# Kernel tuning notes

Measured on AMD Instinct MI355X. Metric: run time of the kernel, lower is better.

The kernel has to match this reference:

```python
import jax, jax.numpy as jnp
import numpy as np

EMBED_DIM = 1024
NUM_HEADS = 16
N_POS = 2048
BATCH = 4


def setup_inputs() -> dict:
    key = jax.random.key(0)
    k_x, k_w1, k_b1, k_wo, k_bo = jax.random.split(key, 5)
    s1 = 1.0 / np.sqrt(EMBED_DIM)
    x = jax.random.normal(k_x, (BATCH, N_POS, EMBED_DIM), dtype=jnp.float32)
    # torch Linear weights stored as [in, out] for x @ W + b
    W_qkv = jax.random.uniform(k_w1, (EMBED_DIM, 3 * EMBED_DIM), dtype=jnp.float32, minval=-s1, maxval=s1)
    b_qkv = jax.random.uniform(k_b1, (3 * EMBED_DIM,), dtype=jnp.float32, minval=-s1, maxval=s1)
    W_o = jax.random.uniform(k_wo, (EMBED_DIM, EMBED_DIM), dtype=jnp.float32, minval=-s1, maxval=s1)
    b_o = jax.random.uniform(k_bo, (EMBED_DIM,), dtype=jnp.float32, minval=-s1, maxval=s1)
    return {"x": x, "W_qkv": W_qkv, "b_qkv": b_qkv, "W_o": W_o, "b_o": b_o}


def reference(x, W_qkv, b_qkv, W_o, b_o):
    B, N, C = x.shape
    H = NUM_HEADS
    d_k = C // H
    qkv = x @ W_qkv + b_qkv                       # [B, N, 3C]
    q, k, v = jnp.split(qkv, 3, axis=-1)
    q = q.reshape(B, N, H, d_k).transpose(0, 2, 1, 3)  # [B, H, N, d_k]
    k = k.reshape(B, N, H, d_k).transpose(0, 2, 1, 3)
    v = v.reshape(B, N, H, d_k).transpose(0, 2, 1, 3)
    scores = jnp.einsum('bhqd,bhkd->bhqk', q, k) * (1.0 / np.sqrt(d_k))
    causal = jnp.tril(jnp.ones((N, N), dtype=bool))
    scores = jnp.where(causal, scores, -jnp.inf)
    attn = jax.nn.softmax(scores, axis=-1)
    out = jnp.einsum('bhqk,bhkd->bhqd', attn, v)  # [B, H, N, d_k]
    out = out.transpose(0, 2, 1, 3).reshape(B, N, C)
    return out @ W_o + b_o
```

## Files before the change

### kernel.cpp

```cpp
#include <hip/hip_runtime.h>
#include <hip/hip_bf16.h>

typedef __attribute__((ext_vector_type(8))) __bf16 bf16x8;
typedef __attribute__((ext_vector_type(4))) float f32x4;
typedef __attribute__((ext_vector_type(16))) float f32x16;
typedef __attribute__((ext_vector_type(4))) unsigned short u16x4;
typedef __attribute__((ext_vector_type(8))) unsigned short u16x8;
typedef __attribute__((ext_vector_type(4))) unsigned int u32x4;
typedef unsigned short u16;

#define MFMA16 __builtin_amdgcn_mfma_f32_16x16x32_bf16
#define MFMA32 __builtin_amdgcn_mfma_f32_32x32x16_bf16

#if __has_builtin(__builtin_amdgcn_exp2f)
#define EXP2F __builtin_amdgcn_exp2f
#else
#define EXP2F(x) __expf((x) * 0.69314718056f)
#endif

__device__ inline u16 f32_to_bf16_bits(float f) {
    unsigned u = __builtin_bit_cast(unsigned, f);
    unsigned r = u + 0x7FFFu + ((u >> 16) & 1u);
    return (u16)(r >> 16);
}

__device__ inline void g2l16(const void* g, void* l) {
    __builtin_amdgcn_global_load_lds(
        (const __attribute__((address_space(1))) unsigned int*)g,
        (__attribute__((address_space(3))) unsigned int*)l,
        16, 0, 0);
}

__device__ inline float red32_max(float x) { return fmaxf(x, __shfl_xor(x, 32)); }
__device__ inline float red32_sum(float x) { return x + __shfl_xor(x, 32); }

__global__ void cvt_bf16_kernel(const float* __restrict__ in, u16* __restrict__ out, int n) {
    int i = (blockIdx.x * 256 + threadIdx.x) * 8;
    if (i >= n) return;
    f32x4 v0 = *(const f32x4*)&in[i];
    f32x4 v1 = *(const f32x4*)&in[i + 4];
    u16x8 r;
#pragma unroll
    for (int j = 0; j < 4; ++j) {
        r[j] = f32_to_bf16_bits(v0[j]);
        r[j + 4] = f32_to_bf16_bits(v1[j]);
    }
    *(u16x8*)&out[i] = r;
}

__global__ __launch_bounds__(256) void cvt_t2_kernel(
    const float* __restrict__ W1, u16* __restrict__ WT1, int N1,
    const float* __restrict__ W2, u16* __restrict__ WT2, int N2, int K)
{
    int bx = blockIdx.x;
    const float* W; u16* WT; int N;
    const int nb1 = N1 >> 6;
    if (bx < nb1) { W = W1; WT = WT1; N = N1; }
    else          { W = W2; WT = WT2; N = N2; bx -= nb1; }
    const int w = threadIdx.x >> 6, l = threadIdx.x & 63;
    const int n = bx * 64 + l;
    const int k0 = blockIdx.y * 32 + w * 8;
    u16x8 r;
#pragma unroll
    for (int i = 0; i < 8; ++i)
        r[i] = f32_to_bf16_bits(W[(size_t)(k0 + i) * N + n]);
    *(u16x8*)&WT[(size_t)n * K + k0] = r;
}

template <int STORE_BF16>
__global__ __launch_bounds__(256) void gemm_nt(
    const u16* __restrict__ A, const u16* __restrict__ BT,
    const float* __restrict__ bias, void* __restrict__ Cv,
    int M, int N, int K, int qcols, float qscale, int nbx)
{
    __shared__ __align__(16) u16 SM[24576];
    const int tid = threadIdx.x;
    const int w = tid >> 6, l = tid & 63;
    const int lr = l & 15, lh = l >> 4;
    const int wr = (w >> 1) * 64, wc = (w & 1) * 64;

    const int xcd = blockIdx.x & 7;
    const int j = blockIdx.x >> 3;
    const int g = j >> 5;
    const int r = j & 31;
    const int m0 = (xcd * 8 + (r >> 2)) * 128;
    const int n0 = (g * 4 + (r & 3)) * 128;
    (void)nbx;

    const int NT = K >> 5;

    const int f0 = tid, f1 = 256 + tid;
    const int r0 = f0 >> 2, r1 = f1 >> 2;
    const int cs0 = ((f0 & 3) ^ ((r0 >> 1) & 3)) * 8;
    const int cs1 = ((f1 & 3) ^ ((r1 >> 1) & 3)) * 8;
    const size_t arow0 = (size_t)(m0 + r0) * K, arow1 = (size_t)(m0 + r1) * K;
    const size_t brow0 = (size_t)(n0 + r0) * K, brow1 = (size_t)(n0 + r1) * K;

#define STAGE_TILE(t, set)                                                     \
    do {                                                                       \
        const int kk_ = (t) * 32;                                              \
        u16* dst_ = SM + (set) * 8192 + w * 512;                               \
        g2l16(A + arow0 + kk_ + cs0, dst_);                                    \
        g2l16(BT + brow0 + kk_ + cs0, dst_ + 4096);                            \
        g2l16(A + arow1 + kk_ + cs1, dst_ + 2048);                             \
        g2l16(BT + brow1 + kk_ + cs1, dst_ + 4096 + 2048);                     \
    } while (0)

    f32x4 acc[4][4];
#pragma unroll
    for (int m = 0; m < 4; ++m)
#pragma unroll
        for (int n = 0; n < 4; ++n) acc[m][n] = (f32x4)(0.0f);

    STAGE_TILE(0, 0);
    STAGE_TILE(1, 1);
    asm volatile("s_waitcnt vmcnt(4) lgkmcnt(0)\n\ts_barrier" ::: "memory");

    const int csw = (lr >> 1) & 3;
    int s0 = 0, s2 = 2;
    for (int t = 0; t < NT; ++t) {
        if (t + 2 < NT) STAGE_TILE(t + 2, s2);

        const u16* As = SM + s0 * 8192;
        const u16* Bs = As + 4096;
        bf16x8 af[4], bfr[4];
#pragma unroll
        for (int m = 0; m < 4; ++m)
            af[m] = *(const bf16x8*)&As[(wr + m * 16 + lr) * 32 + ((lh ^ csw) << 3)];
#pragma unroll
        for (int n = 0; n < 4; ++n)
            bfr[n] = *(const bf16x8*)&Bs[(wc + n * 16 + lr) * 32 + ((lh ^ csw) << 3)];
        __builtin_amdgcn_s_setprio(1);
#pragma unroll
        for (int m = 0; m < 4; ++m)
#pragma unroll
            for (int n = 0; n < 4; ++n)
                acc[m][n] = MFMA16(af[m], bfr[n], acc[m][n], 0, 0, 0);
        __builtin_amdgcn_s_setprio(0);

        if (t + 2 < NT)
            asm volatile("s_waitcnt vmcnt(4) lgkmcnt(0)\n\ts_barrier" ::: "memory");
        else if (t + 1 < NT)
            asm volatile("s_waitcnt vmcnt(0) lgkmcnt(0)\n\ts_barrier" ::: "memory");

        s0 = (s0 == 2) ? 0 : s0 + 1;
        s2 = (s2 == 2) ? 0 : s2 + 1;
    }
#undef STAGE_TILE

#pragma unroll
    for (int m = 0; m < 4; ++m) {
        int row = m0 + wr + m * 16 + lh * 4;
#pragma unroll
        for (int n = 0; n < 4; ++n) {
            int col = n0 + wc + n * 16 + lr;
            float bs = bias[col];
            float sc = (col < qcols) ? qscale : 1.0f;
#pragma unroll
            for (int j2 = 0; j2 < 4; ++j2) {
                float v = (acc[m][n][j2] + bs) * sc;
                if (STORE_BF16)
                    ((u16*)Cv)[(size_t)(row + j2) * N + col] = f32_to_bf16_bits(v);
                else
                    ((float*)Cv)[(size_t)(row + j2) * N + col] = v;
            }
        }
    }
}

__global__ __launch_bounds__(512, 1) void attn_kernel(
    const u16* __restrict__ qkv, u16* __restrict__ ctx)
{
    __shared__ __align__(16) u16 SM[32768];

    const int bid = blockIdx.x;
    const int xcd = bid & 7, jj = bid >> 3;
    const int bh = xcd * 8 + (jj >> 2);
    const int pr = jj & 3;
    const int b = bh >> 4, h = bh & 15;
    const size_t rowbase = (size_t)b * 2048;
    const int tid = threadIdx.x, w = tid >> 6, l = tid & 63;
    const int lq = l & 31, lk = l >> 5;

    const int rsub = l >> 3;
    const int cstage = l & 7;
    const int kchunk = cstage ^ rsub;

    bf16x8 vreg[2];

#pragma unroll
    for (int pass = 0; pass < 2; ++pass) {
        const int qt = pass ? (7 - pr) : pr;
        const int q0 = qt * 256;
        const int nt = 2 * qt + 2;
        const int qbase = q0 + w * 32;

        const u16* qp = qkv + (rowbase + qbase + lq) * 3072 + h * 64 + lk * 8;
        bf16x8 qf[4];
#pragma unroll
        for (int j = 0; j < 4; ++j) qf[j] = *(const bf16x8*)(qp + j * 16);

        f32x16 ot[2];
#pragma unroll
        for (int dt = 0; dt < 2; ++dt) ot[dt] = (f32x16)(0.0f);
        float m_run = -3e38f, l_run = 0.0f;

        __syncthreads();
#pragma unroll
        for (int p = 0; p < 2; ++p) {
            const int r = w * 16 + p * 8 + rsub;
            g2l16(qkv + (rowbase + r) * 3072 + 1024 + h * 64 + kchunk * 8,
                  SM + w * 1024 + p * 512);
            vreg[p] = *(const bf16x8*)(qkv + (rowbase + r) * 3072 + 2048 + h * 64 + cstage * 8);
        }
        asm volatile("s_waitcnt vmcnt(0)" ::: "memory");
#pragma unroll
        for (int p = 0; p < 2; ++p) {
            const int r = w * 16 + p * 8 + rsub;
#pragma unroll
            for (int i = 0; i < 8; ++i) {
                const int d = cstage * 8 + i;
                SM[16384 + ((d * 128 + r) ^ (((i ^ cstage) & 7) << 3))] = ((const u16*)&vreg[p])[i];
            }
        }
        __syncthreads();

        for (int t = 0; t < nt; ++t) {
            const int c = t & 1;
            const int kb = t * 128;
            u16* const Kb = SM + (c ? 8192 : 0);
            u16* const Vb = SM + 16384 + (c ? 8192 : 0);

            if (t + 1 < nt) {
                const int kb2 = kb + 128;
#pragma unroll
                for (int p = 0; p < 2; ++p) {
                    const int r = w * 16 + p * 8 + rsub;
                    g2l16(qkv + (rowbase + kb2 + r) * 3072 + 1024 + h * 64 + kchunk * 8,
                          SM + (c ? 0 : 8192) + w * 1024 + p * 512);
                    vreg[p] = *(const bf16x8*)(qkv + (rowbase + kb2 + r) * 3072 + 2048 + h * 64 + cstage * 8);
                }
            }

            if (kb <= qbase + 31) {
                bf16x8 kf[4][4];
#pragma unroll
                for (int kt = 0; kt < 4; ++kt)
#pragma unroll
                    for (int j = 0; j < 4; ++j)
                        kf[kt][j] = *(const bf16x8*)&Kb[((kt * 32 + lq) * 64 + j * 16 + lk * 8) ^ ((lq & 7) << 3)];

                f32x16 sf[4];
                __builtin_amdgcn_s_setprio(1);
#pragma unroll
                for (int kt = 0; kt < 4; ++kt) {
                    f32x16 z = (f32x16)(0.0f);
#pragma unroll
                    for (int j = 0; j < 4; ++j) z = MFMA32(kf[kt][j], qf[j], z, 0, 0, 0);
                    sf[kt] = z;
                }
                __builtin_amdgcn_s_setprio(0);

                float mt = -3e38f;
                if (kb + 127 > qbase) {
                    const int qrow = qbase + lq;
#pragma unroll
                    for (int kt = 0; kt < 4; ++kt)
#pragma unroll
                        for (int r = 0; r < 16; ++r) {
                            const int key = kb + kt * 32 + (r & 3) + 8 * (r >> 2) + 4 * lk;
                            float v = sf[kt][r];
                            if (key > qrow) v = -3e38f;
                            sf[kt][r] = v;
                            mt = fmaxf(mt, v);
                        }
                } else {
#pragma unroll
                    for (int kt = 0; kt < 4; ++kt)
#pragma unroll
                        for (int r = 0; r < 16; ++r) mt = fmaxf(mt, sf[kt][r]);
                }
                mt = red32_max(mt);

                const bool defer = __all(mt <= m_run + 16.0f);
                float mn = m_run;
                if (!defer) {
                    mn = fmaxf(m_run, mt);
                    const float alpha = EXP2F(m_run - mn);
                    m_run = mn;
                    l_run *= alpha;
#pragma unroll
                    for (int dt = 0; dt < 2; ++dt)
#pragma unroll
                        for (int r = 0; r < 16; ++r) ot[dt][r] *= alpha;
                }
                float rs = 0.0f;
#pragma unroll
                for (int kt = 0; kt < 4; ++kt)
#pragma unroll
                    for (int r = 0; r < 16; ++r) {
                        const float pp = EXP2F(sf[kt][r] - mn);
                        sf[kt][r] = pp;
                        rs += pp;
                    }
                l_run += red32_sum(rs);

                unsigned pc[4][4][2];
#pragma unroll
                for (int kt = 0; kt < 4; ++kt)
#pragma unroll
                    for (int rg = 0; rg < 4; ++rg) {
                        unsigned d0, d1;
                        asm("v_cvt_pk_bf16_f32 %0, %1, %2"
                            : "=v"(d0) : "v"((float)sf[kt][rg * 4 + 0]), "v"((float)sf[kt][rg * 4 + 1]));
                        asm("v_cvt_pk_bf16_f32 %0, %1, %2"
                            : "=v"(d1) : "v"((float)sf[kt][rg * 4 + 2]), "v"((float)sf[kt][rg * 4 + 3]));
                        pc[kt][rg][0] = d0;
                        pc[kt][rg][1] = d1;
                    }

                __builtin_amdgcn_s_setprio(1);
#pragma unroll
                for (int kt = 0; kt < 4; ++kt)
#pragma unroll
                    for (int hh = 0; hh < 2; ++hh) {
                        unsigned a0 = pc[kt][2 * hh][0], a1 = pc[kt][2 * hh][1];
                        unsigned b0 = pc[kt][2 * hh + 1][0], b1 = pc[kt][2 * hh + 1][1];
                        asm("v_permlane32_swap_b32 %0, %1" : "+v"(a0), "+v"(b0));
                        asm("v_permlane32_swap_b32 %0, %1" : "+v"(a1), "+v"(b1));
                        u32x4 wv = {a0, a1, b0, b1};
                        const bf16x8 pb = __builtin_bit_cast(bf16x8, wv);
                        const int k0 = 2 * kt + hh;
#pragma unroll
                        for (int dt = 0; dt < 2; ++dt) {
                            const int d = dt * 32 + lq;
                            const int vswz = ((d & 7) ^ (d >> 3)) & 7;
                            const bf16x8 vf = *(const bf16x8*)&Vb[((d * 128) + (k0 * 16 + lk * 8)) ^ (vswz << 3)];
                            ot[dt] = MFMA32(vf, pb, ot[dt], 0, 0, 0);
                        }
                    }
                __builtin_amdgcn_s_setprio(0);
            }

            asm volatile("s_waitcnt vmcnt(0)" ::: "memory");
            if (t + 1 < nt) {
                u16* const Vn = SM + 16384 + (c ? 0 : 8192);
#pragma unroll
                for (int p = 0; p < 2; ++p) {
                    const int r = w * 16 + p * 8 + rsub;
#pragma unroll
                    for (int i = 0; i < 8; ++i) {
                        const int d = cstage * 8 + i;
                        Vn[((d * 128 + r) ^ (((i ^ cstage) & 7) << 3))] = ((const u16*)&vreg[p])[i];
                    }
                }
            }
            __syncthreads();
        }

        u16* const out_l = SM + w * 2176;
        const float inv = 1.0f / l_run;
#pragma unroll
        for (int dt = 0; dt < 2; ++dt)
#pragma unroll
            for (int r = 0; r < 16; ++r) {
                const int d = dt * 32 + (r & 3) + 8 * (r >> 2) + 4 * lk;
                out_l[lq * 68 + d] = f32_to_bf16_bits(ot[dt][r] * inv);
            }
#pragma unroll
        for (int rr = 0; rr < 4; ++rr) {
            const int row = rr * 8 + (l >> 3);
            const bf16x8 v = *(const bf16x8*)&out_l[row * 68 + (l & 7) * 8];
            *(bf16x8*)(ctx + (rowbase + qbase + row) * 1024 + h * 64 + (l & 7) * 8) = v;
        }
    }
}

extern "C" void kernel_launch(void* const* d_in, const int* in_sizes, int n_in,
                              void* d_out, int out_size, void* d_ws, size_t ws_size,
                              hipStream_t stream) {
    const float* x      = (const float*)d_in[0];
    const float* W_qkv  = (const float*)d_in[1];
    const float* b_qkv  = (const float*)d_in[2];
    const float* W_o    = (const float*)d_in[3];
    const float* b_o    = (const float*)d_in[4];
    float* out = (float*)d_out;

    const int M = 4 * 2048;
    const int C = 1024;
    u16* qkv   = (u16*)d_ws;
    u16* xb    = qkv   + (size_t)M * 3 * C;
    u16* wqkvt = xb    + (size_t)M * C;
    u16* ctx   = wqkvt + (size_t)3 * C * C;
    u16* wot   = ctx   + (size_t)M * C;

    const float SCQ = 0.125f * 1.44269504089f;

    cvt_bf16_kernel<<<(M * C) / (256 * 8), 256, 0, stream>>>(x, xb, M * C);
    cvt_t2_kernel<<<dim3(3 * C / 64 + C / 64, C / 32), 256, 0, stream>>>(
        W_qkv, wqkvt, 3 * C, W_o, wot, C, C);

    gemm_nt<1><<<(3 * C / 128) * (M / 128), 256, 0, stream>>>(xb, wqkvt, b_qkv, qkv,
                                                              M, 3 * C, C, C, SCQ, 3 * C / 128);

    attn_kernel<<<256, 512, 0, stream>>>(qkv, ctx);

    gemm_nt<0><<<(C / 128) * (M / 128), 256, 0, stream>>>(ctx, wot, b_o, out,
                                                          M, C, C, 0, 1.0f, C / 128);
}
```

Baseline: 161.9 us.

## Add 8-wave 128x256 tiled GEMM with chunked staging for QKV projection

Adds a new QKV projection GEMM that uses 512 threads (8 waves) and a 128x256 output tile, double-buffered in 96KB of LDS. Global-to-LDS copies are split into three chunks that are interleaved with two MFMA phases, with explicit barriers and wave priority bumps around the MFMA blocks. The wider N tile is meant to increase reuse of the A tile and reduce global traffic, while the pipelining hides load latency. The cost is more LDS per block and extra barriers, which may lower occupancy.

```diff
diff --git a/kernel.cpp b/kernel.cpp
--- a/kernel.cpp
+++ b/kernel.cpp
@@ -68,6 +68,134 @@
 }
 
 template <int STORE_BF16>
+__global__ __launch_bounds__(512) void gemm_8p2(
+    const u16* __restrict__ A, const u16* __restrict__ BT,
+    const float* __restrict__ bias, void* __restrict__ Cv,
+    int M, int N, int K, int qcols, float qscale)
+{
+    __shared__ __align__(16) u16 SM[49152];
+    const int tid = threadIdx.x;
+    const int w = tid >> 6, l = tid & 63;
+    const int lr = l & 15, lh = l >> 4;
+    const int wr = (w >> 2) * 64;
+    const int wc = (w & 3) * 64;
+
+    const int xcd = blockIdx.x & 7;
+    const int jb = blockIdx.x >> 3;
+    const int g = jb >> 4;
+    const int r = jb & 15;
+    const int m0 = (xcd * 8 + (r >> 1)) * 128;
+    const int n0 = (g * 2 + (r & 1)) * 256;
+
+    const int NT = K >> 6;
+
+    const int f0 = tid, f1 = 512 + tid;
+    const int r0 = f0 >> 3, r1 = f1 >> 3;
+    const int c0 = ((f0 & 7) ^ (r0 & 7)) * 8;
+
+#define STAGE_CHUNK(j, c)                                                       \
+    do {                                                                        \
+        const int kk_ = (j) * 64;                                               \
+        u16* db_ = SM + (((j) & 1) * 24576) + (c) * 8192;                       \
+        const u16* base_ = ((c) == 0) ? (A + (size_t)m0 * K)                    \
+                                      : (BT + (size_t)(n0 + ((c)-1) * 128) * K);\
+        g2l16(base_ + (size_t)r0 * K + kk_ + c0, db_ + f0 * 8);                 \
+        g2l16(base_ + (size_t)r1 * K + kk_ + c0, db_ + f1 * 8);                 \
+    } while (0)
+
+    f32x4 acc[4][4];
+#pragma unroll
+    for (int m = 0; m < 4; ++m)
+#pragma unroll
+        for (int n = 0; n < 4; ++n) acc[m][n] = (f32x4)(0.0f);
+
+    STAGE_CHUNK(0, 0); STAGE_CHUNK(0, 1); STAGE_CHUNK(0, 2);
+
+    const int swk = lr & 7;
+    for (int j = 0; j < NT; ++j) {
+        const u16* Ab = SM + (j & 1) * 24576;
+        const u16* Bb = Ab + 8192;
+
+        if (j + 1 < NT) {
+            STAGE_CHUNK(j + 1, 0);
+            asm volatile("s_waitcnt vmcnt(2)\n\ts_barrier" ::: "memory");
+        } else {
+            asm volatile("s_waitcnt vmcnt(0)\n\ts_barrier" ::: "memory");
+        }
+
+        bf16x8 af[4][2], bfr[2][2];
+#pragma unroll
+        for (int m = 0; m < 4; ++m) {
+            const int row = wr + m * 16 + lr;
+#pragma unroll
+            for (int ks = 0; ks < 2; ++ks)
+                af[m][ks] = *(const bf16x8*)&Ab[row * 64 + (((ks * 4 + lh) ^ swk) << 3)];
+        }
+#pragma unroll
+        for (int n = 0; n < 2; ++n) {
+            const int row = wc + n * 16 + lr;
+#pragma unroll
+            for (int ks = 0; ks < 2; ++ks)
+                bfr[n][ks] = *(const bf16x8*)&Bb[row * 64 + (((ks * 4 + lh) ^ swk) << 3)];
+        }
+        if (j + 1 < NT) STAGE_CHUNK(j + 1, 1);
+
+        asm volatile("s_barrier\n\ts_waitcnt lgkmcnt(0)" ::: "memory");
+        __builtin_amdgcn_s_setprio(1);
+#pragma unroll
+        for (int m = 0; m < 4; ++m)
+#pragma unroll
+            for (int n = 0; n < 2; ++n)
+#pragma unroll
+                for (int ks = 0; ks < 2; ++ks)
+                    acc[m][n] = MFMA16(af[m][ks], bfr[n][ks], acc[m][n], 0, 0, 0);
+        __builtin_amdgcn_s_setprio(0);
+        asm volatile("s_barrier" ::: "memory");
+
+#pragma unroll
+        for (int n = 0; n < 2; ++n) {
+            const int row = wc + (n + 2) * 16 + lr;
+#pragma unroll
+            for (int ks = 0; ks < 2; ++ks)
+                bfr[n][ks] = *(const bf16x8*)&Bb[row * 64 + (((ks * 4 + lh) ^ swk) << 3)];
+        }
+        if (j + 1 < NT) STAGE_CHUNK(j + 1, 2);
+
+        asm volatile("s_barrier\n\ts_waitcnt lgkmcnt(0)" ::: "memory");
+        __builtin_amdgcn_s_setprio(1);
+#pragma unroll
+        for (int m = 0; m < 4; ++m)
+#pragma unroll
+            for (int n = 0; n < 2; ++n)
+#pragma unroll
+                for (int ks = 0; ks < 2; ++ks)
+                    acc[m][n + 2] = MFMA16(af[m][ks], bfr[n][ks], acc[m][n + 2], 0, 0, 0);
+        __builtin_amdgcn_s_setprio(0);
+        asm volatile("s_barrier" ::: "memory");
+    }
+#undef STAGE_CHUNK
+
+#pragma unroll
+    for (int m = 0; m < 4; ++m) {
+        int row = m0 + wr + m * 16 + lh * 4;
+#pragma unroll
+        for (int n = 0; n < 4; ++n) {
+            int col = n0 + wc + n * 16 + lr;
+            float bs = bias[col];
+            float sc = (col < qcols) ? qscale : 1.0f;
+#pragma unroll
+            for (int j2 = 0; j2 < 4; ++j2) {
+                float v = (acc[m][n][j2] + bs) * sc;
+                if (STORE_BF16)
+                    ((u16*)Cv)[(size_t)(row + j2) * N + col] = f32_to_bf16_bits(v);
+                else
+                    ((float*)Cv)[(size_t)(row + j2) * N + col] = v;
+            }
+        }
+    }
+}
+
+template <int STORE_BF16>
 __global__ __launch_bounds__(256) void gemm_nt(
     const u16* __restrict__ A, const u16* __restrict__ BT,
     const float* __restrict__ bias, void* __restrict__ Cv,
@@ -400,8 +528,8 @@
     cvt_t2_kernel<<<dim3(3 * C / 64 + C / 64, C / 32), 256, 0, stream>>>(
         W_qkv, wqkvt, 3 * C, W_o, wot, C, C);
 
-    gemm_nt<1><<<(3 * C / 128) * (M / 128), 256, 0, stream>>>(xb, wqkvt, b_qkv, qkv,
-                                                              M, 3 * C, C, C, SCQ, 3 * C / 128);
+    gemm_8p2<1><<<(M / 128) * (3 * C / 256), 512, 0, stream>>>(xb, wqkvt, b_qkv, qkv,
+                                                               M, 3 * C, C, C, SCQ);
 
     attn_kernel<<<256, 512, 0, stream>>>(qkv, ctx);
 
```

Result: no change. 160.7 us (-0.8%).
